# Kernel optimization log

Measured on AMD Instinct MI355X. Metric: run time of the kernel, lower is better.

## Reference

```python
import jax, jax.numpy as jnp
import numpy as np

ALPHA = 0.25
GAMMA = 2.0
EPS = 1e-4


def setup_inputs() -> dict:
    key = jax.random.key(0)
    ks = jax.random.split(key, 10)
    B, A, C, M = 8, 49104, 80, 32
    classifications = jax.random.uniform(ks[0], (B, A, C), dtype=jnp.float32,
                                         minval=1e-3, maxval=1.0 - 1e-3)
    regressions = jax.random.normal(ks[1], (B, A, 4), dtype=jnp.float32) * 0.1
    # anchors in yxyx layout (code uses col1=x1, col0=y1, col3=x2, col2=y2)
    ay1 = jax.random.uniform(ks[2], (A,), dtype=jnp.float32) * 440.0
    ax1 = jax.random.uniform(ks[3], (A,), dtype=jnp.float32) * 440.0
    ah = jax.random.uniform(ks[4], (A,), dtype=jnp.float32) * 96.0 + 8.0
    aw = jax.random.uniform(ks[5], (A,), dtype=jnp.float32) * 96.0 + 8.0
    anchors = jnp.stack([ay1, ax1, ay1 + ah, ax1 + aw], axis=1)[None]  # [1,A,4]
    # annotations: xyxy + class label, all valid (class >= 0)
    gx1 = jax.random.uniform(ks[6], (B, M), dtype=jnp.float32) * 400.0
    gy1 = jax.random.uniform(ks[7], (B, M), dtype=jnp.float32) * 400.0
    gw = jax.random.uniform(ks[8], (B, M), dtype=jnp.float32) * 100.0 + 4.0
    gh = jax.random.uniform(ks[9], (B, M), dtype=jnp.float32) * 100.0 + 4.0
    labels = jax.random.randint(jax.random.fold_in(key, 99), (B, M), 0, C).astype(jnp.float32)
    annotations = jnp.stack([gx1, gy1, gx1 + gw, gy1 + gh, labels], axis=-1)  # [B,M,5]
    return {"classifications": classifications, "regressions": regressions,
            "anchors": anchors, "annotations": annotations}


def _focal_loss(classifications, regressions, anchors, annotations):
    anchor = anchors[0]                                   # [A,4] yxyx
    a_w = anchor[:, 3] - anchor[:, 1]
    a_h = anchor[:, 2] - anchor[:, 0]
    a_cx = anchor[:, 1] + 0.5 * a_w
    a_cy = anchor[:, 0] + 0.5 * a_h
    xa1, ya1 = anchor[:, 1:2], anchor[:, 0:1]             # [A,1]
    xa2, ya2 = anchor[:, 3:4], anchor[:, 2:3]
    area_a = (xa2 - xa1) * (ya2 - ya1)                    # [A,1]

    def per_image(cls, reg, ann):
        boxes = ann[:, :4]                                # [M,4] xyxy
        labels = ann[:, 4].astype(jnp.int32)              # [M]
        xb1, yb1, xb2, yb2 = boxes[:, 0], boxes[:, 1], boxes[:, 2], boxes[:, 3]
        area_b = (xb2 - xb1) * (yb2 - yb1)                # [M]
        iw = jnp.clip(jnp.minimum(xa2, xb2) - jnp.maximum(xa1, xb1), 0.0)
        ih = jnp.clip(jnp.minimum(ya2, yb2) - jnp.maximum(ya1, yb1), 0.0)
        inter = iw * ih                                   # [A,M]
        iou = inter / (area_a + area_b - inter)
        iou_max = jnp.max(iou, axis=1)                    # [A]
        iou_arg = jnp.argmax(iou, axis=1)                 # [A]

        cls = jnp.clip(cls, EPS, 1.0 - EPS)               # [A,C]
        pos = iou_max >= 0.5
        neg = iou_max < 0.4
        one_hot = jax.nn.one_hot(labels[iou_arg], cls.shape[1], dtype=cls.dtype)
        # -1 = ignore (0.4 <= IoU < 0.5), 0 = background, one-hot for positives
        targets = jnp.where(pos[:, None], one_hot,
                            jnp.where(neg[:, None], 0.0, -1.0))
        alpha_f = jnp.where(targets == 1.0, ALPHA, 1.0 - ALPHA)
        fw = jnp.where(targets == 1.0, 1.0 - cls, cls)
        fw = alpha_f * fw ** GAMMA
        bce = -(targets * jnp.log(cls) + (1.0 - targets) * jnp.log(1.0 - cls))
        cls_loss = jnp.where(targets != -1.0, fw * bce, 0.0)
        num_pos = jnp.sum(pos).astype(cls.dtype)
        cls_l = jnp.sum(cls_loss) / jnp.maximum(num_pos, 1.0)

        ab = boxes[iou_arg]                               # [A,4]
        g_w = ab[:, 2] - ab[:, 0]
        g_h = ab[:, 3] - ab[:, 1]
        g_cx = ab[:, 0] + 0.5 * g_w                       # centers from unclamped wh (matches torch)
        g_cy = ab[:, 1] + 0.5 * g_h
        g_w = jnp.clip(g_w, 1.0)
        g_h = jnp.clip(g_h, 1.0)
        tdx = (g_cx - a_cx) / a_w
        tdy = (g_cy - a_cy) / a_h
        tdw = jnp.log(g_w / a_w)
        tdh = jnp.log(g_h / a_h)
        reg_t = jnp.stack([tdy, tdx, tdh, tdw], axis=1)   # [A,4]
        diff = jnp.abs(reg_t - reg)
        sl1 = jnp.where(diff <= 1.0 / 9.0, 0.5 * 9.0 * diff ** 2, diff - 0.5 / 9.0)
        sl1 = jnp.where(pos[:, None], sl1, 0.0)
        reg_l = jnp.where(num_pos > 0,
                          jnp.sum(sl1) / jnp.maximum(num_pos * 4.0, 1.0), 0.0)
        return cls_l, reg_l

    cls_ls, reg_ls = jax.vmap(per_image)(classifications, regressions, annotations)
    return jnp.mean(cls_ls, keepdims=True), jnp.mean(reg_ls, keepdims=True)


def reference(classifications, regressions, anchors, annotations):
    return _focal_loss(classifications, regressions, anchors, annotations)
```

## Files before the change

### kernel.cpp

```cpp
#include <hip/hip_runtime.h>

#define NCLS 80
#define NQ   20
#define NBOX 32
#define CHUNK 256
#define LN2_075 0.5198603854199589

__global__ __launch_bounds__(256) void focal_main(
    const float* __restrict__ cls,
    const float* __restrict__ reg,
    const float* __restrict__ anchors,
    const float* __restrict__ ann,
    float4* __restrict__ slots,
    int A, int nbx)
{
    __shared__ float4 s_box[NBOX];
    __shared__ float  s_area[NBOX];
    __shared__ float  s_label[NBOX];
    __shared__ float  s_red[4][4];

    const int b    = blockIdx.y;
    const int tid  = threadIdx.x;
    const int base = blockIdx.x * CHUNK;
    const int a    = base + tid;

    if (tid < NBOX) {
        const float* p = ann + (size_t)b * NBOX * 5 + tid * 5;
        const float4 bx = make_float4(p[0], p[1], p[2], p[3]);
        s_box[tid]   = bx;
        s_area[tid]  = (bx.z - bx.x) * (bx.w - bx.y);
        s_label[tid] = p[4];
    }
    __syncthreads();

    float reg_acc = 0.f, pos_acc = 0.f, corr = 0.f;
    if (a < A) {
        const float4 an = *(const float4*)(anchors + (size_t)a * 4);
        const float ya1 = an.x, xa1 = an.y, ya2 = an.z, xa2 = an.w;
        const float area_a = (xa2 - xa1) * (ya2 - ya1);

        float4 b0 = s_box[0];
        float iw = fmaxf(fminf(xa2, b0.z) - fmaxf(xa1, b0.x), 0.f);
        float ih = fmaxf(fminf(ya2, b0.w) - fmaxf(ya1, b0.y), 0.f);
        float ib = iw * ih;
        float ub = area_a + s_area[0] - ib;
        int   arg = 0;
        #pragma unroll
        for (int mm = 1; mm < NBOX; ++mm) {
            const float4 bm = s_box[mm];
            iw = fmaxf(fminf(xa2, bm.z) - fmaxf(xa1, bm.x), 0.f);
            ih = fmaxf(fminf(ya2, bm.w) - fmaxf(ya1, bm.y), 0.f);
            const float im = iw * ih;
            const float um = area_a + s_area[mm] - im;
            const bool gt = (im * ub) > (ib * um);
            ib  = gt ? im : ib;
            ub  = gt ? um : ub;
            arg = gt ? mm : arg;
        }
        const float iou_max = ib / ub;

        if (iou_max >= 0.5f) {
            pos_acc = 1.f;
            const float4 bb = s_box[arg];
            const int L = (int)s_label[arg];
            const float c = cls[((size_t)b * A + a) * NCLS + L];
            corr = 0.25f * (1.f - c) * (1.f - c) * (-__logf(c))
                 - 0.75f * c * c * (-__logf(1.f - c));
            float gw = bb.z - bb.x, gh = bb.w - bb.y;
            const float gcx = bb.x + 0.5f * gw, gcy = bb.y + 0.5f * gh;
            gw = fmaxf(gw, 1.f); gh = fmaxf(gh, 1.f);
            const float aw = xa2 - xa1, ah = ya2 - ya1;
            const float acx = xa1 + 0.5f * aw, acy = ya1 + 0.5f * ah;
            const float t0 = (gcy - acy) / ah;
            const float t1 = (gcx - acx) / aw;
            const float t2 = __logf(gh / ah);
            const float t3 = __logf(gw / aw);
            const float4 rg = *(const float4*)(reg + ((size_t)b * A + a) * 4);
            const float d[4] = { fabsf(t0 - rg.x), fabsf(t1 - rg.y),
                                 fabsf(t2 - rg.z), fabsf(t3 - rg.w) };
            const float TH = 1.f / 9.f, HB = 0.5f / 9.f;
            #pragma unroll
            for (int k = 0; k < 4; ++k)
                reg_acc += (d[k] <= TH) ? 4.5f * d[k] * d[k] : d[k] - HB;
        } else if (iou_max >= 0.4f) {
            const float4* crow = (const float4*)(cls + ((size_t)b * A + a) * NCLS);
            float neg = 0.f;
            #pragma unroll 5
            for (int q = 0; q < NQ; ++q) {
                const float4 v = crow[q];
                neg = fmaf(v.x * v.x, __log2f(1.f - v.x), neg);
                neg = fmaf(v.y * v.y, __log2f(1.f - v.y), neg);
                neg = fmaf(v.z * v.z, __log2f(1.f - v.z), neg);
                neg = fmaf(v.w * v.w, __log2f(1.f - v.w), neg);
            }
            corr = (float)LN2_075 * neg;
        }
    }

    float S0 = 0.f, S1 = 0.f;
    const float4* cbase = (const float4*)(cls + ((size_t)b * A + base) * NCLS);
    if (base + CHUNK <= A) {
        #pragma unroll
        for (int g = 0; g < 2; ++g) {
            float4 v[10];
            #pragma unroll
            for (int i = 0; i < 10; ++i)
                v[i] = cbase[tid + ((g * 10 + i) << 8)];
            #pragma unroll
            for (int i = 0; i < 10; ++i) {
                const float4 w = v[i];
                S0 = fmaf(w.x * w.x, __log2f(1.f - w.x), S0);
                S1 = fmaf(w.y * w.y, __log2f(1.f - w.y), S1);
                S0 = fmaf(w.z * w.z, __log2f(1.f - w.z), S0);
                S1 = fmaf(w.w * w.w, __log2f(1.f - w.w), S1);
            }
        }
    } else {
        const int nq = (A - base) * NQ;
        for (int i = 0; i < NQ; ++i) {
            const int j = tid + (i << 8);
            if (j < nq) {
                const float4 w = cbase[j];
                S0 = fmaf(w.x * w.x, __log2f(1.f - w.x), S0);
                S1 = fmaf(w.y * w.y, __log2f(1.f - w.y), S1);
                S0 = fmaf(w.z * w.z, __log2f(1.f - w.z), S0);
                S1 = fmaf(w.w * w.w, __log2f(1.f - w.w), S1);
            }
        }
    }
    float S = S0 + S1;

    #pragma unroll
    for (int off = 32; off; off >>= 1) {
        S       += __shfl_xor(S,       off, 64);
        corr    += __shfl_xor(corr,    off, 64);
        reg_acc += __shfl_xor(reg_acc, off, 64);
        pos_acc += __shfl_xor(pos_acc, off, 64);
    }
    if ((tid & 63) == 0) {
        const int w = tid >> 6;
        s_red[w][0] = S; s_red[w][1] = corr;
        s_red[w][2] = reg_acc; s_red[w][3] = pos_acc;
    }
    __syncthreads();
    if (tid == 0) {
        float St = 0.f, Ct = 0.f, Rt = 0.f, Pt = 0.f;
        #pragma unroll
        for (int w = 0; w < 4; ++w) {
            St += s_red[w][0]; Ct += s_red[w][1];
            Rt += s_red[w][2]; Pt += s_red[w][3];
        }
        slots[(size_t)b * nbx + blockIdx.x] = make_float4(St, Ct, Rt, Pt);
    }
}

__global__ __launch_bounds__(256) void focal_finalize(
    const float4* __restrict__ slots,
    float* __restrict__ out, int nbx, int B)
{
    __shared__ double s_acc[8][4];
    const int tid = threadIdx.x;
    const int g = tid >> 5;
    const int l = tid & 31;
    double cm = 0.0, rm = 0.0;
    for (int b0 = 0; b0 < B; b0 += 8) {
        const int b = b0 + g;
        float sx = 0.f, sy = 0.f, sz = 0.f, sw = 0.f;
        if (b < B) {
            for (int k = l; k < nbx; k += 32) {
                const float4 s = slots[(size_t)b * nbx + k];
                sx += s.x; sy += s.y; sz += s.z; sw += s.w;
            }
        }
        #pragma unroll
        for (int off = 16; off; off >>= 1) {
            sx += __shfl_xor(sx, off, 64);
            sy += __shfl_xor(sy, off, 64);
            sz += __shfl_xor(sz, off, 64);
            sw += __shfl_xor(sw, off, 64);
        }
        if (l == 0 && b < B) {
            s_acc[g][0] = sx; s_acc[g][1] = sy;
            s_acc[g][2] = sz; s_acc[g][3] = sw;
        }
        __syncthreads();
        if (tid == 0) {
            for (int gg = 0; gg < 8 && b0 + gg < B; ++gg) {
                const double St = s_acc[gg][0], Ct = s_acc[gg][1];
                const double Rt = s_acc[gg][2], np = s_acc[gg][3];
                cm += (Ct - LN2_075 * St) / fmax(np, 1.0);
                rm += (np > 0.0) ? Rt / fmax(np * 4.0, 1.0) : 0.0;
            }
        }
        __syncthreads();
    }
    if (tid == 0) {
        out[0] = (float)(cm / B);
        out[1] = (float)(rm / B);
    }
}

extern "C" void kernel_launch(void* const* d_in, const int* in_sizes, int n_in,
                              void* d_out, int out_size, void* d_ws, size_t ws_size,
                              hipStream_t stream) {
    const float* cls     = (const float*)d_in[0];
    const float* reg     = (const float*)d_in[1];
    const float* anchors = (const float*)d_in[2];
    const float* ann     = (const float*)d_in[3];
    float* out = (float*)d_out;

    const int A = in_sizes[2] / 4;
    const int B = in_sizes[1] / (A * 4);

    const int nbx = (A + CHUNK - 1) / CHUNK;
    float4* slots = (float4*)d_ws;

    dim3 g1(nbx, B);
    focal_main<<<g1, 256, 0, stream>>>(cls, reg, anchors, ann, slots, A, nbx);
    focal_finalize<<<1, 256, 0, stream>>>(slots, out, nbx, B);
}
```

Before: 37.55 us.

## Use 512-thread blocks over 384 anchors and prefetch class rows before IoU

Each block now has 512 threads and covers 384 anchors, so the dense class-row sum is split across more threads and each thread handles 15 float4 loads instead of 20. The first five loads are issued before the IoU matching loop so their memory latency overlaps with the box-matching math. Only the first 384 threads do anchor matching, which leaves the other 128 threads idle during that phase. The launch bound now requests 8 blocks per multiprocessor, which may put pressure on register allocation.

```diff
diff --git a/kernel.cpp b/kernel.cpp
--- a/kernel.cpp
+++ b/kernel.cpp
@@ -3,10 +3,12 @@
 #define NCLS 80
 #define NQ   20
 #define NBOX 32
-#define CHUNK 256
+#define NTHR 512
+#define CHUNK 384
+#define QPT   15
 #define LN2_075 0.5198603854199589
 
-__global__ __launch_bounds__(256) void focal_main(
+__global__ __launch_bounds__(NTHR, 8) void focal_main(
     const float* __restrict__ cls,
     const float* __restrict__ reg,
     const float* __restrict__ anchors,
@@ -17,12 +19,12 @@
     __shared__ float4 s_box[NBOX];
     __shared__ float  s_area[NBOX];
     __shared__ float  s_label[NBOX];
-    __shared__ float  s_red[4][4];
+    __shared__ float  s_red[8][4];
 
     const int b    = blockIdx.y;
     const int tid  = threadIdx.x;
     const int base = blockIdx.x * CHUNK;
-    const int a    = base + tid;
+    const bool full = (base + CHUNK <= A);
 
     if (tid < NBOX) {
         const float* p = ann + (size_t)b * NBOX * 5 + tid * 5;
@@ -33,8 +35,17 @@
     }
     __syncthreads();
 
+    const float4* cbase = (const float4*)(cls + ((size_t)b * A + base) * NCLS);
+
+    float4 v0[5];
+    if (full) {
+        #pragma unroll
+        for (int i = 0; i < 5; ++i) v0[i] = cbase[tid + i * NTHR];
+    }
+
     float reg_acc = 0.f, pos_acc = 0.f, corr = 0.f;
-    if (a < A) {
+    const int a = base + tid;
+    if (tid < CHUNK && a < A) {
         const float4 an = *(const float4*)(anchors + (size_t)a * 4);
         const float ya1 = an.x, xa1 = an.y, ya2 = an.z, xa2 = an.w;
         const float area_a = (xa2 - xa1) * (ya2 - ya1);
@@ -98,16 +109,23 @@
     }
 
     float S0 = 0.f, S1 = 0.f;
-    const float4* cbase = (const float4*)(cls + ((size_t)b * A + base) * NCLS);
-    if (base + CHUNK <= A) {
-        #pragma unroll
-        for (int g = 0; g < 2; ++g) {
-            float4 v[10];
+    if (full) {
+        #pragma unroll
+        for (int i = 0; i < 5; ++i) {
+            const float4 w = v0[i];
+            S0 = fmaf(w.x * w.x, __log2f(1.f - w.x), S0);
+            S1 = fmaf(w.y * w.y, __log2f(1.f - w.y), S1);
+            S0 = fmaf(w.z * w.z, __log2f(1.f - w.z), S0);
+            S1 = fmaf(w.w * w.w, __log2f(1.f - w.w), S1);
+        }
+        #pragma unroll
+        for (int g = 1; g < 3; ++g) {
+            float4 v[5];
             #pragma unroll
-            for (int i = 0; i < 10; ++i)
-                v[i] = cbase[tid + ((g * 10 + i) << 8)];
+            for (int i = 0; i < 5; ++i)
+                v[i] = cbase[tid + (g * 5 + i) * NTHR];
             #pragma unroll
-            for (int i = 0; i < 10; ++i) {
+            for (int i = 0; i < 5; ++i) {
                 const float4 w = v[i];
                 S0 = fmaf(w.x * w.x, __log2f(1.f - w.x), S0);
                 S1 = fmaf(w.y * w.y, __log2f(1.f - w.y), S1);
@@ -117,8 +135,8 @@
         }
     } else {
         const int nq = (A - base) * NQ;
-        for (int i = 0; i < NQ; ++i) {
-            const int j = tid + (i << 8);
+        for (int i = 0; i < QPT; ++i) {
+            const int j = tid + i * NTHR;
             if (j < nq) {
                 const float4 w = cbase[j];
                 S0 = fmaf(w.x * w.x, __log2f(1.f - w.x), S0);
@@ -146,7 +164,7 @@
     if (tid == 0) {
         float St = 0.f, Ct = 0.f, Rt = 0.f, Pt = 0.f;
         #pragma unroll
-        for (int w = 0; w < 4; ++w) {
+        for (int w = 0; w < 8; ++w) {
             St += s_red[w][0]; Ct += s_red[w][1];
             Rt += s_red[w][2]; Pt += s_red[w][3];
         }
@@ -216,6 +234,6 @@
     float4* slots = (float4*)d_ws;
 
     dim3 g1(nbx, B);
-    focal_main<<<g1, 256, 0, stream>>>(cls, reg, anchors, ann, slots, A, nbx);
+    focal_main<<<g1, NTHR, 0, stream>>>(cls, reg, anchors, ann, slots, A, nbx);
     focal_finalize<<<1, 256, 0, stream>>>(slots, out, nbx, B);
 }
```

New measurement: 95.89 us. 2.55x slower.
